# Optimization experiments

Hardware: AMD Instinct MI355X
Metric: run time of the kernel (lower is better)

The kernel has to match this reference:

```python
import jax, jax.numpy as jnp
import numpy as np

B, D, NCLS = 65536, 784, 10

def sparse_layer(x, idx, w, b):
    # x: [B, D]; idx: [Dout, k] int; w: [Dout, k]; b: [Dout]
    # out[b, n] = sum_j x[b, idx[n, j]] * w[n, j] + b[n]
    g = x[:, idx]                      # [B, Dout, k] gather
    return jnp.einsum('bnk,nk->bn', g, w) + b

def setup_inputs() -> dict:
    key = jax.random.key(0)
    ks = jax.random.split(key, 12)
    def rn(k, shape, scale):
        return jax.random.normal(k, shape, dtype=jnp.float32) * scale
    return {
        'x': rn(ks[0], (B, D), 1.0),
        'idx1': jax.random.randint(ks[1], (D, 2), 0, D, dtype=jnp.int32),
        'w1': rn(ks[2], (D, 2), 0.5),
        'b1': rn(ks[3], (D,), 0.1),
        'idx2': jax.random.randint(ks[4], (D, 4), 0, D, dtype=jnp.int32),
        'w2': rn(ks[5], (D, 4), 0.4),
        'b2': rn(ks[6], (D,), 0.1),
        'idx3': jax.random.randint(ks[7], (D, 8), 0, D, dtype=jnp.int32),
        'w3': rn(ks[8], (D, 8), 0.3),
        'b3': rn(ks[9], (D,), 0.1),
        'fc_w': rn(ks[10], (NCLS, D), 0.05),
        'fc_b': rn(ks[11], (NCLS,), 0.05),
    }

def reference(x, idx1, w1, b1, idx2, w2, b2, idx3, w3, b3, fc_w, fc_b):
    h = jax.nn.gelu(sparse_layer(x, idx1, w1, b1), approximate=False)
    h = jax.nn.gelu(sparse_layer(h, idx2, w2, b2), approximate=False)
    h = jax.nn.gelu(sparse_layer(h, idx3, w3, b3), approximate=False)
    logits = h @ fc_w.T + fc_b          # [B, 10]
    return jax.nn.softmax(logits, axis=-1)
```

## Files before the change

kernel.cpp:

```cpp
#include <hip/hip_runtime.h>

#define D_    784
#define ROWS  8
#define NCLS  10
#define BLOCK 256
#define NB    (65536 / ROWS)
#define HSTR  12

__device__ __forceinline__ float gelu_f(float x) {
    float x2    = x * x;
    float inner = fmaf(0.044715f * x, x2, x);
    float e     = exp2f(2.3022082f * inner);
    float r     = __builtin_amdgcn_rcpf(e + 1.0f);
    return fmaf(-x, r, x);
}

__device__ __forceinline__ void fma4(float4& a, const float4& h4, float wk) {
    a.x = fmaf(h4.x, wk, a.x);
    a.y = fmaf(h4.y, wk, a.y);
    a.z = fmaf(h4.z, wk, a.z);
    a.w = fmaf(h4.w, wk, a.w);
}

template <int K>
__device__ __forceinline__ void loadIdxW(const int* __restrict__ idx,
                                         const float* __restrict__ w,
                                         int n, int* jc, float* wc) {
    if constexpr (K == 2) {
        int2   j = *(const int2*)(idx + n * 2);
        float2 v = *(const float2*)(w + n * 2);
        jc[0] = j.x; jc[1] = j.y; wc[0] = v.x; wc[1] = v.y;
    } else if constexpr (K == 4) {
        int4   j = *(const int4*)(idx + n * 4);
        float4 v = *(const float4*)(w + n * 4);
        jc[0] = j.x; jc[1] = j.y; jc[2] = j.z; jc[3] = j.w;
        wc[0] = v.x; wc[1] = v.y; wc[2] = v.z; wc[3] = v.w;
    } else {
        int4   ja = *(const int4*)(idx + n * 8);
        int4   jb = *(const int4*)(idx + n * 8 + 4);
        float4 va = *(const float4*)(w + n * 8);
        float4 vb = *(const float4*)(w + n * 8 + 4);
        jc[0] = ja.x; jc[1] = ja.y; jc[2] = ja.z; jc[3] = ja.w;
        jc[4] = jb.x; jc[5] = jb.y; jc[6] = jb.z; jc[7] = jb.w;
        wc[0] = va.x; wc[1] = va.y; wc[2] = va.z; wc[3] = va.w;
        wc[4] = vb.x; wc[5] = vb.y; wc[6] = vb.z; wc[7] = vb.w;
    }
}

template <int K>
__device__ __forceinline__ void layer_fn(const float* __restrict__ src,
                                         float* __restrict__ dst,
                                         const int* __restrict__ idx,
                                         const float* __restrict__ w,
                                         const float* __restrict__ bias,
                                         int tid) {
    int   jc[K];
    float wc[K];
    float bc;
    loadIdxW<K>(idx, w, tid, jc, wc);
    bc = bias[tid];
#pragma unroll 1
    for (int i = 0; i < 4; ++i) {
        int n  = tid + 256 * i;
        int nn = n + 256;
        int   jn[K]; float wn[K]; float bn = 0.f;
#pragma unroll
        for (int k = 0; k < K; ++k) { jn[k] = 0; wn[k] = 0.f; }
        if (nn < D_) {
            loadIdxW<K>(idx, w, nn, jn, wn);
            bn = bias[nn];
        }
        if (n < D_) {
            float4 aL = make_float4(bc, bc, bc, bc);
            float4 aH = make_float4(bc, bc, bc, bc);
#pragma unroll
            for (int k = 0; k < K; ++k) {
                const float* hb = src + jc[k] * HSTR;
                float4 h0 = *(const float4*)(hb);
                float4 h1 = *(const float4*)(hb + 4);
                fma4(aL, h0, wc[k]);
                fma4(aH, h1, wc[k]);
            }
            float* db = dst + n * HSTR;
            *(float4*)(db)     = make_float4(gelu_f(aL.x), gelu_f(aL.y),
                                             gelu_f(aL.z), gelu_f(aL.w));
            *(float4*)(db + 4) = make_float4(gelu_f(aH.x), gelu_f(aH.y),
                                             gelu_f(aH.z), gelu_f(aH.w));
        }
#pragma unroll
        for (int k = 0; k < K; ++k) { jc[k] = jn[k]; wc[k] = wn[k]; }
        bc = bn;
    }
    __syncthreads();
}

__global__ __launch_bounds__(BLOCK)
void circnn_kernel(const float* __restrict__ x,
                   const int* __restrict__ idx1, const float* __restrict__ w1, const float* __restrict__ b1,
                   const int* __restrict__ idx2, const float* __restrict__ w2, const float* __restrict__ b2,
                   const int* __restrict__ idx3, const float* __restrict__ w3, const float* __restrict__ b3,
                   const float* __restrict__ fcw, const float* __restrict__ fcb,
                   float* __restrict__ out) {
    __shared__ __align__(16) float bufA[D_ * HSTR];
    __shared__ __align__(16) float bufB[D_ * HSTR];
    __shared__ float logits[ROWS * NCLS];

    const int tid  = threadIdx.x;
    const int row0 = blockIdx.x * ROWS;

    const float* xb = x + (size_t)row0 * D_;
#pragma unroll 1
    for (int i = 0; i < 4; ++i) {
        int n = tid + 256 * i;
        if (n < D_) {
            float4 v0, v1;
            v0.x = xb[0 * D_ + n]; v0.y = xb[1 * D_ + n];
            v0.z = xb[2 * D_ + n]; v0.w = xb[3 * D_ + n];
            v1.x = xb[4 * D_ + n]; v1.y = xb[5 * D_ + n];
            v1.z = xb[6 * D_ + n]; v1.w = xb[7 * D_ + n];
            float* db = bufA + n * HSTR;
            *(float4*)(db)     = v0;
            *(float4*)(db + 4) = v1;
        }
    }
    __syncthreads();

    layer_fn<2>(bufA, bufB, idx1, w1, b1, tid);
    layer_fn<4>(bufB, bufA, idx2, w2, b2, tid);
    layer_fn<8>(bufA, bufB, idx3, w3, b3, tid);

    float4* part4 = (float4*)bufA;
    if (tid < 128) {
        const int jj = tid >> 1;
        const int qq = tid & 1;
        float4 facc[NCLS];
#pragma unroll
        for (int c = 0; c < NCLS; ++c) facc[c] = make_float4(0.f, 0.f, 0.f, 0.f);
#pragma unroll 1
        for (int i = 0; i < 13; ++i) {
            int n = jj + 64 * i;
            if (n < D_) {
                float4 hv = *(const float4*)(bufB + n * HSTR + qq * 4);
#pragma unroll
                for (int c = 0; c < NCLS; ++c)
                    fma4(facc[c], hv, fcw[c * D_ + n]);
            }
        }
#pragma unroll
        for (int c = 0; c < NCLS; ++c)
            part4[(jj * 2 + qq) * NCLS + c] = facc[c];
    }
    __syncthreads();

    if (tid < ROWS * NCLS) {
        int r = tid / NCLS, c = tid - r * NCLS;
        int qq = r >> 2, comp = r & 3;
        const float* pf = (const float*)part4;
        float s = fcb[c];
#pragma unroll 4
        for (int jj = 0; jj < 64; ++jj)
            s += pf[((jj * 2 + qq) * NCLS + c) * 4 + comp];
        logits[tid] = s;
    }
    __syncthreads();

    if (tid < ROWS * NCLS) {
        int r = tid / NCLS;
        const float* lg = logits + r * NCLS;
        float m = lg[0];
#pragma unroll
        for (int c = 1; c < NCLS; ++c) m = fmaxf(m, lg[c]);
        float s = 0.f;
#pragma unroll
        for (int c = 0; c < NCLS; ++c) s += __expf(lg[c] - m);
        out[(size_t)row0 * NCLS + tid] = __expf(logits[tid] - m) / s;
    }
}

extern "C" void kernel_launch(void* const* d_in, const int* in_sizes, int n_in,
                              void* d_out, int out_size, void* d_ws, size_t ws_size,
                              hipStream_t stream) {
    const float* x    = (const float*)d_in[0];
    const int*   idx1 = (const int*)d_in[1];
    const float* w1   = (const float*)d_in[2];
    const float* b1   = (const float*)d_in[3];
    const int*   idx2 = (const int*)d_in[4];
    const float* w2   = (const float*)d_in[5];
    const float* b2   = (const float*)d_in[6];
    const int*   idx3 = (const int*)d_in[7];
    const float* w3   = (const float*)d_in[8];
    const float* b3   = (const float*)d_in[9];
    const float* fcw  = (const float*)d_in[10];
    const float* fcb  = (const float*)d_in[11];
    float* out = (float*)d_out;

    circnn_kernel<<<dim3(NB), dim3(BLOCK), 0, stream>>>(
        x, idx1, w1, b1, idx2, w2, b2, idx3, w3, b3, fcw, fcb, out);
}
```

Baseline: 486.0 us.

## Use one thread per neuron with 832-thread blocks and unpadded LDS stride

Raises the block size from 256 to 832 threads so each thread handles exactly one of the 784 neurons per layer, dropping the four-iteration loop and its software-prefetched index/weight registers. The LDS row stride shrinks from 12 to 8 floats, cutting shared memory per block from about 75 KB to about 50 KB, which may let more blocks share a CU. The stride-8 layout can add LDS bank conflicts on the random gathers, and 48 of the 832 threads sit idle in each layer.

```diff
diff --git a/kernel.cpp b/kernel.cpp
--- a/kernel.cpp
+++ b/kernel.cpp
@@ -3,9 +3,9 @@
 #define D_    784
 #define ROWS  8
 #define NCLS  10
-#define BLOCK 256
+#define BLOCK 832
 #define NB    (65536 / ROWS)
-#define HSTR  12
+#define HSTR  8
 
 __device__ __forceinline__ float gelu_f(float x) {
     float x2    = x * x;
@@ -23,78 +23,41 @@
 }
 
 template <int K>
-__device__ __forceinline__ void loadIdxW(const int* __restrict__ idx,
-                                         const float* __restrict__ w,
-                                         int n, int* jc, float* wc) {
-    if constexpr (K == 2) {
-        int2   j = *(const int2*)(idx + n * 2);
-        float2 v = *(const float2*)(w + n * 2);
-        jc[0] = j.x; jc[1] = j.y; wc[0] = v.x; wc[1] = v.y;
-    } else if constexpr (K == 4) {
-        int4   j = *(const int4*)(idx + n * 4);
-        float4 v = *(const float4*)(w + n * 4);
-        jc[0] = j.x; jc[1] = j.y; jc[2] = j.z; jc[3] = j.w;
-        wc[0] = v.x; wc[1] = v.y; wc[2] = v.z; wc[3] = v.w;
-    } else {
-        int4   ja = *(const int4*)(idx + n * 8);
-        int4   jb = *(const int4*)(idx + n * 8 + 4);
-        float4 va = *(const float4*)(w + n * 8);
-        float4 vb = *(const float4*)(w + n * 8 + 4);
-        jc[0] = ja.x; jc[1] = ja.y; jc[2] = ja.z; jc[3] = ja.w;
-        jc[4] = jb.x; jc[5] = jb.y; jc[6] = jb.z; jc[7] = jb.w;
-        wc[0] = va.x; wc[1] = va.y; wc[2] = va.z; wc[3] = va.w;
-        wc[4] = vb.x; wc[5] = vb.y; wc[6] = vb.z; wc[7] = vb.w;
-    }
-}
-
-template <int K>
 __device__ __forceinline__ void layer_fn(const float* __restrict__ src,
                                          float* __restrict__ dst,
                                          const int* __restrict__ idx,
                                          const float* __restrict__ w,
                                          const float* __restrict__ bias,
                                          int tid) {
-    int   jc[K];
-    float wc[K];
-    float bc;
-    loadIdxW<K>(idx, w, tid, jc, wc);
-    bc = bias[tid];
-#pragma unroll 1
-    for (int i = 0; i < 4; ++i) {
-        int n  = tid + 256 * i;
-        int nn = n + 256;
-        int   jn[K]; float wn[K]; float bn = 0.f;
+    if (tid < D_) {
+        float bv = bias[tid];
+        float4 aL = make_float4(bv, bv, bv, bv);
+        float4 aH = make_float4(bv, bv, bv, bv);
 #pragma unroll
-        for (int k = 0; k < K; ++k) { jn[k] = 0; wn[k] = 0.f; }
-        if (nn < D_) {
-            loadIdxW<K>(idx, w, nn, jn, wn);
-            bn = bias[nn];
+        for (int k2 = 0; k2 < K / 2; ++k2) {
+            int2   j  = *(const int2*)(idx + tid * K + k2 * 2);
+            float2 wv = *(const float2*)(w + tid * K + k2 * 2);
+            const float* p0 = src + j.x * HSTR;
+            const float* p1 = src + j.y * HSTR;
+            float4 a0 = *(const float4*)(p0);
+            float4 a1 = *(const float4*)(p0 + 4);
+            float4 b0 = *(const float4*)(p1);
+            float4 b1 = *(const float4*)(p1 + 4);
+            fma4(aL, a0, wv.x);
+            fma4(aH, a1, wv.x);
+            fma4(aL, b0, wv.y);
+            fma4(aH, b1, wv.y);
         }
-        if (n < D_) {
-            float4 aL = make_float4(bc, bc, bc, bc);
-            float4 aH = make_float4(bc, bc, bc, bc);
-#pragma unroll
-            for (int k = 0; k < K; ++k) {
-                const float* hb = src + jc[k] * HSTR;
-                float4 h0 = *(const float4*)(hb);
-                float4 h1 = *(const float4*)(hb + 4);
-                fma4(aL, h0, wc[k]);
-                fma4(aH, h1, wc[k]);
-            }
-            float* db = dst + n * HSTR;
-            *(float4*)(db)     = make_float4(gelu_f(aL.x), gelu_f(aL.y),
-                                             gelu_f(aL.z), gelu_f(aL.w));
-            *(float4*)(db + 4) = make_float4(gelu_f(aH.x), gelu_f(aH.y),
-                                             gelu_f(aH.z), gelu_f(aH.w));
-        }
-#pragma unroll
-        for (int k = 0; k < K; ++k) { jc[k] = jn[k]; wc[k] = wn[k]; }
-        bc = bn;
+        float* db = dst + tid * HSTR;
+        *(float4*)(db)     = make_float4(gelu_f(aL.x), gelu_f(aL.y),
+                                         gelu_f(aL.z), gelu_f(aL.w));
+        *(float4*)(db + 4) = make_float4(gelu_f(aH.x), gelu_f(aH.y),
+                                         gelu_f(aH.z), gelu_f(aH.w));
     }
     __syncthreads();
 }
 
-__global__ __launch_bounds__(BLOCK)
+__global__ __launch_bounds__(BLOCK, 4)
 void circnn_kernel(const float* __restrict__ x,
                    const int* __restrict__ idx1, const float* __restrict__ w1, const float* __restrict__ b1,
                    const int* __restrict__ idx2, const float* __restrict__ w2, const float* __restrict__ b2,
@@ -108,20 +71,16 @@
     const int tid  = threadIdx.x;
     const int row0 = blockIdx.x * ROWS;
 
-    const float* xb = x + (size_t)row0 * D_;
-#pragma unroll 1
-    for (int i = 0; i < 4; ++i) {
-        int n = tid + 256 * i;
-        if (n < D_) {
-            float4 v0, v1;
-            v0.x = xb[0 * D_ + n]; v0.y = xb[1 * D_ + n];
-            v0.z = xb[2 * D_ + n]; v0.w = xb[3 * D_ + n];
-            v1.x = xb[4 * D_ + n]; v1.y = xb[5 * D_ + n];
-            v1.z = xb[6 * D_ + n]; v1.w = xb[7 * D_ + n];
-            float* db = bufA + n * HSTR;
-            *(float4*)(db)     = v0;
-            *(float4*)(db + 4) = v1;
-        }
+    if (tid < D_) {
+        const float* xb = x + (size_t)row0 * D_ + tid;
+        float4 v0, v1;
+        v0.x = xb[0 * D_]; v0.y = xb[1 * D_];
+        v0.z = xb[2 * D_]; v0.w = xb[3 * D_];
+        v1.x = xb[4 * D_]; v1.y = xb[5 * D_];
+        v1.z = xb[6 * D_]; v1.w = xb[7 * D_];
+        float* db = bufA + tid * HSTR;
+        *(float4*)(db)     = v0;
+        *(float4*)(db + 4) = v1;
     }
     __syncthreads();
 
```

Result: slower. 541.1 us (+11.3%).
